# Kernel optimization log

Measured on AMD Instinct MI355X. Metric: run time of the kernel, lower is better.

The kernel has to match this reference:

```python
import jax, jax.numpy as jnp
import numpy as np

N_NODES = 50000
D_IN = 256
D_OUT = 128
N_POS = 1600000   # positive edges used for GCN aggregation
N_PRED = 500000   # edges to score


def setup_inputs() -> dict:
    key = jax.random.key(0)
    ks = jax.random.split(key, 6)
    x = jax.random.normal(ks[0], (N_NODES, D_IN), dtype=jnp.float32)
    pos_edge_index = jax.random.randint(ks[1], (2, N_POS), 0, N_NODES)
    edge_index = jax.random.randint(ks[2], (2, N_PRED), 0, N_NODES)
    # init_linear: Linear(d_in, d_in); stored as (in, out) so fwd is x @ W1 + b1
    W1 = jax.random.normal(ks[3], (D_IN, D_IN), dtype=jnp.float32) / np.sqrt(D_IN).astype(np.float32)
    b1 = jnp.zeros((D_IN,), dtype=jnp.float32)
    # GCNConv weight (in, out) and bias
    Wc = jax.random.normal(ks[4], (D_IN, D_OUT), dtype=jnp.float32) / np.sqrt(D_IN).astype(np.float32)
    bc = jnp.zeros((D_OUT,), dtype=jnp.float32)
    return dict(x=x, edge_index=edge_index, pos_edge_index=pos_edge_index,
                W1=W1, b1=b1, Wc=Wc, bc=bc)


def reference(x, edge_index, pos_edge_index, W1, b1, Wc, bc):
    n = x.shape[0]
    # init_linear
    h = x @ W1 + b1                                  # [N, D_IN]
    # GCNConv: linear transform first, then normalized scatter-add aggregation
    h = h @ Wc                                       # [N, D_OUT]
    # add self-loops (PyG GCNConv default add_self_loops=True, edge_weight=1)
    loops = jnp.arange(n, dtype=pos_edge_index.dtype)
    row = jnp.concatenate([pos_edge_index[0], loops])  # source
    col = jnp.concatenate([pos_edge_index[1], loops])  # target (aggregation)
    # symmetric normalization: deg over target, norm = d^-1/2[row]*d^-1/2[col]
    deg = jax.ops.segment_sum(jnp.ones_like(col, dtype=h.dtype), col, num_segments=n)
    dinv = jnp.where(deg > 0, jax.lax.rsqrt(deg), 0.0)
    norm = dinv[row] * dinv[col]                     # [E+N]
    msgs = h[row] * norm[:, None]                    # gather + scale
    out = jax.ops.segment_sum(msgs, col, num_segments=n) + bc  # scatter-add + bias
    # edge dot-product scoring
    logits = (out[edge_index[0]] * out[edge_index[1]]).sum(axis=-1)  # [N_PRED]
    return logits
```

## Files before the change

### kernel.cpp

```cpp
#include <hip/hip_runtime.h>

#define N_NODES 50000
#define D_IN 256
#define D_OUT 128
#define N_POS 1600000
#define N_PRED 500000

#define G_BUCKETS 782
#define GPAD 1024
#define SB 640
#define CHUNK 2500
#define CAP 4096
#define GEMM_BLOCKS 782
#define QPRED 125000

#define NT 4
#define TSZ 12500
#define NPB 25
#define AGGB 2000

typedef __attribute__((ext_vector_type(8))) short short8;
typedef __attribute__((ext_vector_type(4))) float f32x4;

__device__ __forceinline__ unsigned short f2bf(float f) {
    unsigned int u = __float_as_uint(f);
    u += 0x7FFFu + ((u >> 16) & 1u);
    return (unsigned short)(u >> 16);
}
__device__ __forceinline__ unsigned int pk2(float a, float b) {
    unsigned int ua = __float_as_uint(a), ub = __float_as_uint(b);
    ua += 0x7FFFu + ((ua >> 16) & 1u);
    ub += 0x7FFFu + ((ub >> 16) & 1u);
    return (ua >> 16) | (ub & 0xFFFF0000u);
}
__device__ __forceinline__ float bflo(unsigned int u) { return __uint_as_float(u << 16); }
__device__ __forceinline__ float bfhi(unsigned int u) { return __uint_as_float(u & 0xFFFF0000u); }

__device__ __forceinline__ float dot8(uint4 ua, uint4 ub) {
    return bflo(ua.x) * bflo(ub.x) + bfhi(ua.x) * bfhi(ub.x)
         + bflo(ua.y) * bflo(ub.y) + bfhi(ua.y) * bfhi(ub.y)
         + bflo(ua.z) * bflo(ub.z) + bfhi(ua.z) * bfhi(ub.z)
         + bflo(ua.w) * bflo(ub.w) + bfhi(ua.w) * bfhi(ub.w);
}

__global__ void fuse_weights_k(const float* __restrict__ W1, const float* __restrict__ Wc,
                               const float* __restrict__ b1,
                               unsigned short* __restrict__ Bp, float* __restrict__ bf,
                               int* __restrict__ bfill) {
    if (blockIdx.x == 128) {
        for (int g = threadIdx.x; g < G_BUCKETS; g += 256) bfill[g] = g * CAP;
        return;
    }
    int gid = blockIdx.x * blockDim.x + threadIdx.x;
    int k = gid >> 7;
    int n = gid & 127;
    float acc = 0.f;
    #pragma unroll 4
    for (int kk = 0; kk < D_IN; ++kk)
        acc += W1[k * D_IN + kk] * Wc[kk * D_OUT + n];
    int ks = k >> 5, q = (k >> 3) & 3, jj = k & 7;
    int nt = n >> 4, nl = n & 15;
    int lane = q * 16 + nl;
    Bp[(((long)(ks * 8 + nt)) * 64 + lane) * 8 + jj] = f2bf(acc);
    if (gid < D_OUT) {
        float accb = 0.f;
        for (int kk = 0; kk < D_IN; ++kk)
            accb += b1[kk] * Wc[kk * D_OUT + gid];
        bf[gid] = accb;
    }
}

__global__ __launch_bounds__(256) void scatter_gemm_k(const int* __restrict__ row,
                                                      const int* __restrict__ col,
                                                      int* __restrict__ bfill,
                                                      unsigned int* __restrict__ eb,
                                                      const float* __restrict__ x,
                                                      const uint4* __restrict__ Bp,
                                                      const float* __restrict__ bf,
                                                      unsigned short* __restrict__ hsb) {
    __shared__ __align__(16) char smem[27456];
    if (blockIdx.x < GEMM_BLOCKS) {
        const int wave = threadIdx.x >> 6;
        const int lane = threadIdx.x & 63;
        const int q    = lane >> 4;
        const int ml   = lane & 15;
        const int m0   = blockIdx.x * 64 + wave * 16;

        f32x4 acc[8];
        #pragma unroll
        for (int t = 0; t < 8; ++t) acc[t] = (f32x4){0.f, 0.f, 0.f, 0.f};

        long arow = m0 + ml; if (arow > N_NODES - 1) arow = N_NODES - 1;
        const float* xrow = x + arow * D_IN + q * 8;

        #pragma unroll
        for (int ks = 0; ks < 8; ++ks) {
            float4 xa = *(const float4*)(xrow + ks * 32);
            float4 xb = *(const float4*)(xrow + ks * 32 + 4);
            union { short8 s; unsigned int u[4]; } af;
            af.u[0] = pk2(xa.x, xa.y);
            af.u[1] = pk2(xa.z, xa.w);
            af.u[2] = pk2(xb.x, xb.y);
            af.u[3] = pk2(xb.z, xb.w);
            #pragma unroll
            for (int nt = 0; nt < 8; ++nt) {
                union { uint4 v; short8 s; } bu;
                bu.v = Bp[(long)(ks * 8 + nt) * 64 + lane];
                acc[nt] = __builtin_amdgcn_mfma_f32_16x16x32_bf16(af.s, bu.s, acc[nt], 0, 0, 0);
            }
        }

        unsigned short* o = (unsigned short*)smem + wave * 2048;
        #pragma unroll
        for (int nt = 0; nt < 8; ++nt) {
            float bn = bf[nt * 16 + ml];
            #pragma unroll
            for (int r = 0; r < 4; ++r) {
                float val = acc[nt][r] + bn;
                o[(q * 4 + r) * 128 + nt * 16 + ml] = f2bf(val);
            }
        }
        __syncthreads();
        #pragma unroll
        for (int i = 0; i < 4; ++i) {
            int fb = i * 1024 + lane * 16;
            int v = m0 + (fb >> 8);
            if (v < N_NODES) {
                uint4 val = *(const uint4*)((const char*)o + fb);
                *(uint4*)((char*)hsb + (long)v * 256 + (fb & 255)) = val;
            }
        }
    } else {
        int* hist  = (int*)smem;
        int* lofs  = hist + GPAD;
        int* fill2 = lofs + GPAD;
        int* base  = fill2 + GPAD;
        int* part  = base + GPAD;
        unsigned int* stag = (unsigned int*)(part + 256);
        int t = threadIdx.x;
        for (int i = t; i < GPAD; i += 256) { hist[i] = 0; fill2[i] = 0; }
        __syncthreads();
        int e0 = (blockIdx.x - GEMM_BLOCKS) * CHUNK;
        for (int i = t; i < CHUNK; i += 256)
            atomicAdd(&hist[col[e0 + i] >> 6], 1);
        __syncthreads();
        int h[4], p4 = 0;
        #pragma unroll
        for (int i = 0; i < 4; ++i) { h[i] = hist[4 * t + i]; p4 += h[i]; }
        part[t] = p4;
        __syncthreads();
        for (int d = 1; d < 256; d <<= 1) {
            int add = (t >= d) ? part[t - d] : 0;
            __syncthreads();
            part[t] += add;
            __syncthreads();
        }
        int ex = part[t] - p4;
        #pragma unroll
        for (int i = 0; i < 4; ++i) { lofs[4 * t + i] = ex; ex += h[i]; }
        __syncthreads();
        for (int g = t; g < G_BUCKETS; g += 256) {
            int c = hist[g];
            base[g] = c ? atomicAdd(&bfill[g], c) : 0;
        }
        for (int i = t; i < CHUNK; i += 256) {
            int c = col[e0 + i];
            int g = c >> 6;
            unsigned int u = (unsigned int)row[e0 + i] | ((unsigned int)(c & 63) << 16)
                           | ((unsigned int)g << 22);
            int lp = atomicAdd(&fill2[g], 1);
            stag[lofs[g] + lp] = u;
        }
        __syncthreads();
        for (int i = t; i < CHUNK; i += 256) {
            unsigned int u = stag[i];
            int g = u >> 22;
            eb[base[g] + (i - lofs[g])] = u;
        }
    }
}

__global__ __launch_bounds__(256) void csr_build_k(const int* __restrict__ bfill,
                                                   const unsigned int* __restrict__ eb,
                                                   unsigned short* __restrict__ csr,
                                                   int* __restrict__ offs5,
                                                   float* __restrict__ dinv) {
    __shared__ unsigned int stag[CAP];
    __shared__ unsigned short stag2[CAP];
    __shared__ int hist[256], lofs[256], fill[256], part[256];
    int t = threadIdx.x;
    int g = blockIdx.x;
    int s = g * CAP;
    int cnt = bfill[g] - s;
    hist[t] = 0; fill[t] = 0;
    __syncthreads();
    for (int i = t; i < cnt; i += 256) {
        unsigned int u = eb[s + i];
        stag[i] = u;
        int r = u & 0xFFFF;
        int tile = (r >= TSZ) + (r >= 2 * TSZ) + (r >= 3 * TSZ);
        atomicAdd(&hist[((u >> 16) & 63) * NT + tile], 1);
    }
    __syncthreads();
    int hv = hist[t];
    part[t] = hv;
    __syncthreads();
    for (int d = 1; d < 256; d <<= 1) {
        int add = (t >= d) ? part[t - d] : 0;
        __syncthreads();
        part[t] += add;
        __syncthreads();
    }
    lofs[t] = part[t] - hv;
    __syncthreads();
    if (t < 64) {
        int v = g * 64 + t;
        if (v < N_NODES) {
            int b4 = t * NT;
            int o0 = s + lofs[b4];
            int c0 = hist[b4], c1 = hist[b4 + 1], c2 = hist[b4 + 2], c3 = hist[b4 + 3];
            offs5[v * 5 + 0] = o0;
            offs5[v * 5 + 1] = o0 + c0;
            offs5[v * 5 + 2] = o0 + c0 + c1;
            offs5[v * 5 + 3] = o0 + c0 + c1 + c2;
            offs5[v * 5 + 4] = o0 + c0 + c1 + c2 + c3;
            dinv[v] = rsqrtf((float)(c0 + c1 + c2 + c3) + 1.0f);
        }
    }
    for (int i = t; i < cnt; i += 256) {
        unsigned int u = stag[i];
        int r = u & 0xFFFF;
        int tile = (r >= TSZ) + (r >= 2 * TSZ) + (r >= 3 * TSZ);
        int key = ((u >> 16) & 63) * NT + tile;
        int lp = atomicAdd(&fill[key], 1);
        stag2[lofs[key] + lp] = (unsigned short)r;
    }
    __syncthreads();
    for (int i = t; i < cnt; i += 256)
        csr[s + i] = stag2[i];
}

__global__ __launch_bounds__(256) void aggregate_csr_k(const int* __restrict__ offs5,
                                                       const unsigned short* __restrict__ csr,
                                                       const uint4* __restrict__ hs4,
                                                       const float* __restrict__ dinv,
                                                       const float* __restrict__ bc,
                                                       uint4* __restrict__ feat4) {
    __shared__ float accs[NPB][128];
    int tid  = threadIdx.x;
    int wave = tid >> 6;
    int lane = tid & 63;
    int grp  = lane >> 4, li = lane & 15;
    int vbase = blockIdx.x * NPB;

    for (int i = tid; i < NPB * 128; i += 256) ((float*)accs)[i] = 0.f;
    __syncthreads();

    #pragma unroll 1
    for (int tt = 0; tt < NT; ++tt) {
        for (int n = wave; n < NPB; n += 4) {
            int v = vbase + n;
            int s0 = offs5[v * 5 + tt], s1 = offs5[v * 5 + tt + 1];
            if (s0 == s1) continue;
            float a[8] = {0.f, 0.f, 0.f, 0.f, 0.f, 0.f, 0.f, 0.f};
            int i = s0 + grp;
            for (; i + 4 < s1; i += 8) {
                int r0 = csr[i], r1 = csr[i + 4];
                uint4 u0 = hs4[r0 * 16 + li];
                uint4 u1 = hs4[r1 * 16 + li];
                float d0 = dinv[r0], d1 = dinv[r1];
                a[0] = fmaf(d0, bflo(u0.x), a[0]); a[0] = fmaf(d1, bflo(u1.x), a[0]);
                a[1] = fmaf(d0, bfhi(u0.x), a[1]); a[1] = fmaf(d1, bfhi(u1.x), a[1]);
                a[2] = fmaf(d0, bflo(u0.y), a[2]); a[2] = fmaf(d1, bflo(u1.y), a[2]);
                a[3] = fmaf(d0, bfhi(u0.y), a[3]); a[3] = fmaf(d1, bfhi(u1.y), a[3]);
                a[4] = fmaf(d0, bflo(u0.z), a[4]); a[4] = fmaf(d1, bflo(u1.z), a[4]);
                a[5] = fmaf(d0, bfhi(u0.z), a[5]); a[5] = fmaf(d1, bfhi(u1.z), a[5]);
                a[6] = fmaf(d0, bflo(u0.w), a[6]); a[6] = fmaf(d1, bflo(u1.w), a[6]);
                a[7] = fmaf(d0, bfhi(u0.w), a[7]); a[7] = fmaf(d1, bfhi(u1.w), a[7]);
            }
            if (i < s1) {
                int r = csr[i];
                uint4 u = hs4[r * 16 + li];
                float d = dinv[r];
                a[0] = fmaf(d, bflo(u.x), a[0]); a[1] = fmaf(d, bfhi(u.x), a[1]);
                a[2] = fmaf(d, bflo(u.y), a[2]); a[3] = fmaf(d, bfhi(u.y), a[3]);
                a[4] = fmaf(d, bflo(u.z), a[4]); a[5] = fmaf(d, bfhi(u.z), a[5]);
                a[6] = fmaf(d, bflo(u.w), a[6]); a[7] = fmaf(d, bfhi(u.w), a[7]);
            }
            #pragma unroll
            for (int j = 0; j < 8; ++j) {
                a[j] += __shfl_xor(a[j], 16);
                a[j] += __shfl_xor(a[j], 32);
            }
            if (grp == 0) {
                #pragma unroll
                for (int j = 0; j < 8; ++j) accs[n][li * 8 + j] += a[j];
            }
        }
    }
    __syncthreads();
    int gid4 = wave * 4 + grp;
    for (int n = gid4; n < NPB; n += 16) {
        int v = vbase + n;
        uint4 su = hs4[(long)v * 16 + li];
        float dv = dinv[v];
        float4 b0 = *(const float4*)(bc + li * 8);
        float4 b1 = *(const float4*)(bc + li * 8 + 4);
        const float* ac = &accs[n][li * 8];
        float f0 = dv * (ac[0] + dv * bflo(su.x)) + b0.x;
        float f1 = dv * (ac[1] + dv * bfhi(su.x)) + b0.y;
        float f2 = dv * (ac[2] + dv * bflo(su.y)) + b0.z;
        float f3 = dv * (ac[3] + dv * bfhi(su.y)) + b0.w;
        float f4 = dv * (ac[4] + dv * bflo(su.z)) + b1.x;
        float f5 = dv * (ac[5] + dv * bfhi(su.z)) + b1.y;
        float f6 = dv * (ac[6] + dv * bflo(su.w)) + b1.z;
        float f7 = dv * (ac[7] + dv * bfhi(su.w)) + b1.w;
        uint4 o;
        o.x = pk2(f0, f1); o.y = pk2(f2, f3); o.z = pk2(f4, f5); o.w = pk2(f6, f7);
        feat4[(long)v * 16 + li] = o;
    }
}

__global__ void score_k(const int* __restrict__ src, const int* __restrict__ dst,
                        const uint4* __restrict__ feat4, float* __restrict__ out) {
    int gid = blockIdx.x * blockDim.x + threadIdx.x;
    int e = gid >> 4;
    int c = gid & 15;
    if (e >= QPRED) return;
    int e0 = e, e1 = e + QPRED, e2 = e + 2 * QPRED, e3 = e + 3 * QPRED;
    int a0 = src[e0], b0 = dst[e0];
    int a1 = src[e1], b1 = dst[e1];
    int a2 = src[e2], b2 = dst[e2];
    int a3 = src[e3], b3 = dst[e3];
    uint4 ua0 = feat4[(long)a0 * 16 + c];
    uint4 ub0 = feat4[(long)b0 * 16 + c];
    uint4 ua1 = feat4[(long)a1 * 16 + c];
    uint4 ub1 = feat4[(long)b1 * 16 + c];
    uint4 ua2 = feat4[(long)a2 * 16 + c];
    uint4 ub2 = feat4[(long)b2 * 16 + c];
    uint4 ua3 = feat4[(long)a3 * 16 + c];
    uint4 ub3 = feat4[(long)b3 * 16 + c];
    float p0 = dot8(ua0, ub0);
    float p1 = dot8(ua1, ub1);
    float p2 = dot8(ua2, ub2);
    float p3 = dot8(ua3, ub3);
    #pragma unroll
    for (int m = 8; m; m >>= 1) {
        p0 += __shfl_xor(p0, m, 16);
        p1 += __shfl_xor(p1, m, 16);
        p2 += __shfl_xor(p2, m, 16);
        p3 += __shfl_xor(p3, m, 16);
    }
    if (c == 0) {
        out[e0] = p0;
        out[e1] = p1;
        out[e2] = p2;
        out[e3] = p3;
    }
}

extern "C" void kernel_launch(void* const* d_in, const int* in_sizes, int n_in,
                              void* d_out, int out_size, void* d_ws, size_t ws_size,
                              hipStream_t stream) {
    const float* x   = (const float*)d_in[0];
    const int*   ei  = (const int*)  d_in[1];
    const int*   pe  = (const int*)  d_in[2];
    const float* W1  = (const float*)d_in[3];
    const float* b1  = (const float*)d_in[4];
    const float* Wc  = (const float*)d_in[5];
    const float* bc  = (const float*)d_in[6];
    float* out = (float*)d_out;

    const int* pe_row = pe;
    const int* pe_col = pe + N_POS;
    const int* ei_src = ei;
    const int* ei_dst = ei + N_PRED;

    char* w = (char*)d_ws;
    unsigned short* Bp = (unsigned short*)w;  w += 32768 * 2;
    float* bf    = (float*)w;                 w += 128 * 4;
    float* dinv  = (float*)w;                 w += 50000 * 4;
    int*   bfill = (int*)w;                   w += GPAD * 4;
    int*   offs5 = (int*)w;                   w += 50000 * 5 * 4;
    unsigned int* eb = (unsigned int*)w;      w += (long)G_BUCKETS * CAP * 4;
    unsigned short* csr = (unsigned short*)w; w += (long)G_BUCKETS * CAP * 2;
    unsigned short* hsb   = (unsigned short*)w;  w += (long)N_NODES * D_OUT * 2;
    unsigned short* featb = (unsigned short*)w;

    fuse_weights_k<<<129, 256, 0, stream>>>(W1, Wc, b1, Bp, bf, bfill);

    scatter_gemm_k<<<GEMM_BLOCKS + SB, 256, 0, stream>>>(pe_row, pe_col, bfill, eb,
                                                         x, (const uint4*)Bp, bf, hsb);

    csr_build_k   <<<G_BUCKETS, 256, 0, stream>>>(bfill, eb, csr, offs5, dinv);

    aggregate_csr_k<<<AGGB, 256, 0, stream>>>(offs5, csr, (const uint4*)hsb,
                                              dinv, bc, (uint4*)featb);

    score_k       <<<(QPRED * 16 + 255) / 256, 256, 0, stream>>>(
                      ei_src, ei_dst, (const uint4*)featb, out);
}
```

Measured before the change: 262.0 us.

## Prescale node features by dinv in CSR build; simplify aggregation to plain sums

The CSR build kernel now multiplies each node's bf16 feature row by its dinv and writes it back, so the aggregation no longer needs a per-neighbour dinv gather and FMA. The aggregation kernel is restructured so each 16-lane group owns two nodes and accumulates in registers, removing the shared-memory accumulators, cross-group shuffles and block sync. Each row is now rounded to bf16 a second time after scaling, and lane groups whose nodes have uneven degree may be imbalanced. It also raises the occupancy hint and changes nodes per block.

```diff
diff --git a/kernel.cpp b/kernel.cpp
--- a/kernel.cpp
+++ b/kernel.cpp
@@ -16,8 +16,8 @@
 
 #define NT 4
 #define TSZ 12500
-#define NPB 25
-#define AGGB 2000
+#define NPB 32
+#define AGGB 1563
 
 typedef __attribute__((ext_vector_type(8))) short short8;
 typedef __attribute__((ext_vector_type(4))) float f32x4;
@@ -184,10 +184,12 @@
                                                    const unsigned int* __restrict__ eb,
                                                    unsigned short* __restrict__ csr,
                                                    int* __restrict__ offs5,
-                                                   float* __restrict__ dinv) {
+                                                   float* __restrict__ dinv,
+                                                   uint4* __restrict__ hsb4) {
     __shared__ unsigned int stag[CAP];
     __shared__ unsigned short stag2[CAP];
     __shared__ int hist[256], lofs[256], fill[256], part[256];
+    __shared__ float dloc[64];
     int t = threadIdx.x;
     int g = blockIdx.x;
     int s = g * CAP;
@@ -215,16 +217,18 @@
     __syncthreads();
     if (t < 64) {
         int v = g * 64 + t;
+        int b4 = t * NT;
+        int c0 = hist[b4], c1 = hist[b4 + 1], c2 = hist[b4 + 2], c3 = hist[b4 + 3];
+        float dl = rsqrtf((float)(c0 + c1 + c2 + c3) + 1.0f);
+        dloc[t] = dl;
         if (v < N_NODES) {
-            int b4 = t * NT;
             int o0 = s + lofs[b4];
-            int c0 = hist[b4], c1 = hist[b4 + 1], c2 = hist[b4 + 2], c3 = hist[b4 + 3];
             offs5[v * 5 + 0] = o0;
             offs5[v * 5 + 1] = o0 + c0;
             offs5[v * 5 + 2] = o0 + c0 + c1;
             offs5[v * 5 + 3] = o0 + c0 + c1 + c2;
             offs5[v * 5 + 4] = o0 + c0 + c1 + c2 + c3;
-            dinv[v] = rsqrtf((float)(c0 + c1 + c2 + c3) + 1.0f);
+            dinv[v] = dl;
         }
     }
     for (int i = t; i < cnt; i += 256) {
@@ -238,86 +242,128 @@
     __syncthreads();
     for (int i = t; i < cnt; i += 256)
         csr[s + i] = stag2[i];
-}
-
-__global__ __launch_bounds__(256) void aggregate_csr_k(const int* __restrict__ offs5,
-                                                       const unsigned short* __restrict__ csr,
-                                                       const uint4* __restrict__ hs4,
-                                                       const float* __restrict__ dinv,
-                                                       const float* __restrict__ bc,
-                                                       uint4* __restrict__ feat4) {
-    __shared__ float accs[NPB][128];
-    int tid  = threadIdx.x;
-    int wave = tid >> 6;
-    int lane = tid & 63;
-    int grp  = lane >> 4, li = lane & 15;
-    int vbase = blockIdx.x * NPB;
-
-    for (int i = tid; i < NPB * 128; i += 256) ((float*)accs)[i] = 0.f;
-    __syncthreads();
+    const int vb = g * 64;
+    for (int i = t; i < 64 * 16; i += 256) {
+        int n = i >> 4;
+        int v = vb + n;
+        if (v < N_NODES) {
+            float d = dloc[n];
+            long idx = (long)v * 16 + (i & 15);
+            uint4 u = hsb4[idx];
+            uint4 o;
+            o.x = pk2(d * bflo(u.x), d * bfhi(u.x));
+            o.y = pk2(d * bflo(u.y), d * bfhi(u.y));
+            o.z = pk2(d * bflo(u.z), d * bfhi(u.z));
+            o.w = pk2(d * bflo(u.w), d * bfhi(u.w));
+            hsb4[idx] = o;
+        }
+    }
+}
+
+__global__ __launch_bounds__(256, 8) void aggregate_csr_k(const int* __restrict__ offs5,
+                                                          const unsigned short* __restrict__ csr,
+                                                          const uint4* __restrict__ hs4,
+                                                          const float* __restrict__ dinv,
+                                                          const float* __restrict__ bc,
+                                                          uint4* __restrict__ feat4) {
+    int tid = threadIdx.x;
+    int li  = tid & 15;
+    int g16 = tid >> 4;
+    int v0 = blockIdx.x * NPB + g16 * 2;
+    int v1 = v0 + 1;
+    bool ok0 = v0 < N_NODES, ok1 = v1 < N_NODES;
+
+    float a0[8] = {0.f, 0.f, 0.f, 0.f, 0.f, 0.f, 0.f, 0.f};
+    float a1[8] = {0.f, 0.f, 0.f, 0.f, 0.f, 0.f, 0.f, 0.f};
 
     #pragma unroll 1
     for (int tt = 0; tt < NT; ++tt) {
-        for (int n = wave; n < NPB; n += 4) {
-            int v = vbase + n;
-            int s0 = offs5[v * 5 + tt], s1 = offs5[v * 5 + tt + 1];
-            if (s0 == s1) continue;
-            float a[8] = {0.f, 0.f, 0.f, 0.f, 0.f, 0.f, 0.f, 0.f};
-            int i = s0 + grp;
-            for (; i + 4 < s1; i += 8) {
-                int r0 = csr[i], r1 = csr[i + 4];
+        if (ok0) {
+            int i  = offs5[v0 * 5 + tt];
+            int s1 = offs5[v0 * 5 + tt + 1];
+            for (; i + 3 < s1; i += 4) {
+                int r0 = csr[i], r1 = csr[i + 1], r2 = csr[i + 2], r3 = csr[i + 3];
                 uint4 u0 = hs4[r0 * 16 + li];
                 uint4 u1 = hs4[r1 * 16 + li];
-                float d0 = dinv[r0], d1 = dinv[r1];
-                a[0] = fmaf(d0, bflo(u0.x), a[0]); a[0] = fmaf(d1, bflo(u1.x), a[0]);
-                a[1] = fmaf(d0, bfhi(u0.x), a[1]); a[1] = fmaf(d1, bfhi(u1.x), a[1]);
-                a[2] = fmaf(d0, bflo(u0.y), a[2]); a[2] = fmaf(d1, bflo(u1.y), a[2]);
-                a[3] = fmaf(d0, bfhi(u0.y), a[3]); a[3] = fmaf(d1, bfhi(u1.y), a[3]);
-                a[4] = fmaf(d0, bflo(u0.z), a[4]); a[4] = fmaf(d1, bflo(u1.z), a[4]);
-                a[5] = fmaf(d0, bfhi(u0.z), a[5]); a[5] = fmaf(d1, bfhi(u1.z), a[5]);
-                a[6] = fmaf(d0, bflo(u0.w), a[6]); a[6] = fmaf(d1, bflo(u1.w), a[6]);
-                a[7] = fmaf(d0, bfhi(u0.w), a[7]); a[7] = fmaf(d1, bfhi(u1.w), a[7]);
-            }
-            if (i < s1) {
+                uint4 u2 = hs4[r2 * 16 + li];
+                uint4 u3 = hs4[r3 * 16 + li];
+                a0[0] += (bflo(u0.x) + bflo(u1.x)) + (bflo(u2.x) + bflo(u3.x));
+                a0[1] += (bfhi(u0.x) + bfhi(u1.x)) + (bfhi(u2.x) + bfhi(u3.x));
+                a0[2] += (bflo(u0.y) + bflo(u1.y)) + (bflo(u2.y) + bflo(u3.y));
+                a0[3] += (bfhi(u0.y) + bfhi(u1.y)) + (bfhi(u2.y) + bfhi(u3.y));
+                a0[4] += (bflo(u0.z) + bflo(u1.z)) + (bflo(u2.z) + bflo(u3.z));
+                a0[5] += (bfhi(u0.z) + bfhi(u1.z)) + (bfhi(u2.z) + bfhi(u3.z));
+                a0[6] += (bflo(u0.w) + bflo(u1.w)) + (bflo(u2.w) + bflo(u3.w));
+                a0[7] += (bfhi(u0.w) + bfhi(u1.w)) + (bfhi(u2.w) + bfhi(u3.w));
+            }
+            for (; i < s1; ++i) {
                 int r = csr[i];
                 uint4 u = hs4[r * 16 + li];
-                float d = dinv[r];
-                a[0] = fmaf(d, bflo(u.x), a[0]); a[1] = fmaf(d, bfhi(u.x), a[1]);
-                a[2] = fmaf(d, bflo(u.y), a[2]); a[3] = fmaf(d, bfhi(u.y), a[3]);
-                a[4] = fmaf(d, bflo(u.z), a[4]); a[5] = fmaf(d, bfhi(u.z), a[5]);
-                a[6] = fmaf(d, bflo(u.w), a[6]); a[7] = fmaf(d, bfhi(u.w), a[7]);
-            }
-            #pragma unroll
-            for (int j = 0; j < 8; ++j) {
-                a[j] += __shfl_xor(a[j], 16);
-                a[j] += __shfl_xor(a[j], 32);
-            }
-            if (grp == 0) {
-                #pragma unroll
-                for (int j = 0; j < 8; ++j) accs[n][li * 8 + j] += a[j];
-            }
-        }
-    }
-    __syncthreads();
-    int gid4 = wave * 4 + grp;
-    for (int n = gid4; n < NPB; n += 16) {
-        int v = vbase + n;
-        uint4 su = hs4[(long)v * 16 + li];
-        float dv = dinv[v];
-        float4 b0 = *(const float4*)(bc + li * 8);
-        float4 b1 = *(const float4*)(bc + li * 8 + 4);
-        const float* ac = &accs[n][li * 8];
-        float f0 = dv * (ac[0] + dv * bflo(su.x)) + b0.x;
-        float f1 = dv * (ac[1] + dv * bfhi(su.x)) + b0.y;
-        float f2 = dv * (ac[2] + dv * bflo(su.y)) + b0.z;
-        float f3 = dv * (ac[3] + dv * bfhi(su.y)) + b0.w;
-        float f4 = dv * (ac[4] + dv * bflo(su.z)) + b1.x;
-        float f5 = dv * (ac[5] + dv * bfhi(su.z)) + b1.y;
-        float f6 = dv * (ac[6] + dv * bflo(su.w)) + b1.z;
-        float f7 = dv * (ac[7] + dv * bfhi(su.w)) + b1.w;
+                a0[0] += bflo(u.x); a0[1] += bfhi(u.x);
+                a0[2] += bflo(u.y); a0[3] += bfhi(u.y);
+                a0[4] += bflo(u.z); a0[5] += bfhi(u.z);
+                a0[6] += bflo(u.w); a0[7] += bfhi(u.w);
+            }
+        }
+        if (ok1) {
+            int i  = offs5[v1 * 5 + tt];
+            int s1 = offs5[v1 * 5 + tt + 1];
+            for (; i + 3 < s1; i += 4) {
+                int r0 = csr[i], r1 = csr[i + 1], r2 = csr[i + 2], r3 = csr[i + 3];
+                uint4 u0 = hs4[r0 * 16 + li];
+                uint4 u1 = hs4[r1 * 16 + li];
+                uint4 u2 = hs4[r2 * 16 + li];
+                uint4 u3 = hs4[r3 * 16 + li];
+                a1[0] += (bflo(u0.x) + bflo(u1.x)) + (bflo(u2.x) + bflo(u3.x));
+                a1[1] += (bfhi(u0.x) + bfhi(u1.x)) + (bfhi(u2.x) + bfhi(u3.x));
+                a1[2] += (bflo(u0.y) + bflo(u1.y)) + (bflo(u2.y) + bflo(u3.y));
+                a1[3] += (bfhi(u0.y) + bfhi(u1.y)) + (bfhi(u2.y) + bfhi(u3.y));
+                a1[4] += (bflo(u0.z) + bflo(u1.z)) + (bflo(u2.z) + bflo(u3.z));
+                a1[5] += (bfhi(u0.z) + bfhi(u1.z)) + (bfhi(u2.z) + bfhi(u3.z));
+                a1[6] += (bflo(u0.w) + bflo(u1.w)) + (bflo(u2.w) + bflo(u3.w));
+                a1[7] += (bfhi(u0.w) + bfhi(u1.w)) + (bfhi(u2.w) + bfhi(u3.w));
+            }
+            for (; i < s1; ++i) {
+                int r = csr[i];
+                uint4 u = hs4[r * 16 + li];
+                a1[0] += bflo(u.x); a1[1] += bfhi(u.x);
+                a1[2] += bflo(u.y); a1[3] += bfhi(u.y);
+                a1[4] += bflo(u.z); a1[5] += bfhi(u.z);
+                a1[6] += bflo(u.w); a1[7] += bfhi(u.w);
+            }
+        }
+    }
+    float4 b0 = *(const float4*)(bc + li * 8);
+    float4 b1 = *(const float4*)(bc + li * 8 + 4);
+    if (ok0) {
+        uint4 su = hs4[(long)v0 * 16 + li];
+        float dv = dinv[v0];
+        float f0 = dv * (a0[0] + bflo(su.x)) + b0.x;
+        float f1 = dv * (a0[1] + bfhi(su.x)) + b0.y;
+        float f2 = dv * (a0[2] + bflo(su.y)) + b0.z;
+        float f3 = dv * (a0[3] + bfhi(su.y)) + b0.w;
+        float f4 = dv * (a0[4] + bflo(su.z)) + b1.x;
+        float f5 = dv * (a0[5] + bfhi(su.z)) + b1.y;
+        float f6 = dv * (a0[6] + bflo(su.w)) + b1.z;
+        float f7 = dv * (a0[7] + bfhi(su.w)) + b1.w;
         uint4 o;
         o.x = pk2(f0, f1); o.y = pk2(f2, f3); o.z = pk2(f4, f5); o.w = pk2(f6, f7);
-        feat4[(long)v * 16 + li] = o;
+        feat4[(long)v0 * 16 + li] = o;
+    }
+    if (ok1) {
+        uint4 su = hs4[(long)v1 * 16 + li];
+        float dv = dinv[v1];
+        float f0 = dv * (a1[0] + bflo(su.x)) + b0.x;
+        float f1 = dv * (a1[1] + bfhi(su.x)) + b0.y;
+        float f2 = dv * (a1[2] + bflo(su.y)) + b0.z;
+        float f3 = dv * (a1[3] + bfhi(su.y)) + b0.w;
+        float f4 = dv * (a1[4] + bflo(su.z)) + b1.x;
+        float f5 = dv * (a1[5] + bfhi(su.z)) + b1.y;
+        float f6 = dv * (a1[6] + bflo(su.w)) + b1.z;
+        float f7 = dv * (a1[7] + bfhi(su.w)) + b1.w;
+        uint4 o;
+        o.x = pk2(f0, f1); o.y = pk2(f2, f3); o.z = pk2(f4, f5); o.w = pk2(f6, f7);
+        feat4[(long)v1 * 16 + li] = o;
     }
 }
 
@@ -392,7 +438,8 @@
     scatter_gemm_k<<<GEMM_BLOCKS + SB, 256, 0, stream>>>(pe_row, pe_col, bfill, eb,
                                                          x, (const uint4*)Bp, bf, hsb);
 
-    csr_build_k   <<<G_BUCKETS, 256, 0, stream>>>(bfill, eb, csr, offs5, dinv);
+    csr_build_k   <<<G_BUCKETS, 256, 0, stream>>>(bfill, eb, csr, offs5, dinv,
+                                                  (uint4*)hsb);
 
     aggregate_csr_k<<<AGGB, 256, 0, stream>>>(offs5, csr, (const uint4*)hsb,
                                               dinv, bc, (uint4*)featb);
```

Result: faster. 238.2 us (-9.1%).
